# Optimization experiments

Measured on AMD Instinct MI355X. Metric: run time of the kernel, lower is better.

## Reference

```python
import jax, jax.numpy as jnp
import numpy as np

B, S, D, H = 2, 2048, 2048, 16
DH = D // H  # 128
EPS = 1e-6


def _rms_norm(x, w):
    # RMSNorm over last dim with learnable scale
    var = jnp.mean(jnp.square(x), axis=-1, keepdims=True)
    return x * jax.lax.rsqrt(var + EPS) * w


def _apply_rope(x, angles):
    # x: [B, S, H, DH]; angles: [S, DH//2]; interleaved pair rotation
    xs = x.reshape(*x.shape[:-1], DH // 2, 2)
    x0, x1 = xs[..., 0], xs[..., 1]
    cos = jnp.cos(angles)[None, :, None, :]  # [1,S,1,DH/2]
    sin = jnp.sin(angles)[None, :, None, :]
    r0 = x0 * cos - x1 * sin
    r1 = x0 * sin + x1 * cos
    return jnp.stack([r0, r1], axis=-1).reshape(x.shape)


def setup_inputs() -> dict:
    key = jax.random.key(0)
    ks = jax.random.split(key, 4)
    x = jax.random.normal(ks[0], (B, S, D), dtype=jnp.float32)
    # standard RoPE angle table: pos * inv_freq
    inv_freq = 1.0 / (10000.0 ** (jnp.arange(0, DH, 2, dtype=jnp.float32) / DH))
    pos = jnp.arange(S, dtype=jnp.float32)
    rp_freqs = pos[:, None] * inv_freq[None, :]  # [S, DH/2]
    Win = jax.random.normal(ks[1], (3 * D, D), dtype=jnp.float32) * (D ** -0.5)
    b_in = jnp.zeros((3 * D,), dtype=jnp.float32)
    Wout = jax.random.normal(ks[2], (D, D), dtype=jnp.float32) * (D ** -0.5)
    b_out = jnp.zeros((D,), dtype=jnp.float32)
    qk_w = jnp.ones((DH,), dtype=jnp.float32)
    out_w = jnp.ones((D,), dtype=jnp.float32)
    return {"x": x, "rp_freqs": rp_freqs, "Win": Win, "b_in": b_in,
            "Wout": Wout, "b_out": b_out, "qk_w": qk_w, "out_w": out_w}


def reference(x, rp_freqs, Win, b_in, Wout, b_out, qk_w, out_w):
    b, s, d = x.shape
    qkv = jnp.einsum('bsd,ed->bse', x, Win) + b_in  # [B,S,3D]
    qkv = qkv.reshape(b, s, 3, H, DH)
    q, k, v = qkv[:, :, 0], qkv[:, :, 1], qkv[:, :, 2]  # each [B,S,H,DH]
    q = _apply_rope(q, rp_freqs)
    k = _apply_rope(k, rp_freqs)
    q = _rms_norm(q, qk_w)
    k = _rms_norm(k, qk_w)
    # causal SDPA, scale = 1/sqrt(DH) (default)
    a = jax.nn.dot_product_attention(q, k, v, is_causal=True)  # [B,S,H,DH]
    a = a.reshape(b, s, d)
    a = _rms_norm(a, out_w)
    return jnp.einsum('bsd,ed->bse', a, Wout) + b_out
```

## Files before the change

### kernel.cpp

```cpp
#include <hip/hip_runtime.h>
#include <cstdint>
#include <cstddef>

#define Bq  2
#define Sq  2048
#define Dq  2048
#define Hq  16
#define DHq 128
#define E3q 6144

typedef __attribute__((ext_vector_type(8))) short s16x8;
typedef __attribute__((ext_vector_type(4))) float f32x4;

__device__ __forceinline__ unsigned short f2bf(float f){
  union { float f; unsigned u; } v; v.f = f;
  unsigned r = v.u + 0x7FFFu + ((v.u >> 16) & 1u);
  return (unsigned short)(r >> 16);
}
__device__ __forceinline__ float bf2f(unsigned short b){
  union { unsigned u; float f; } v; v.u = ((unsigned)b) << 16;
  return v.f;
}
__device__ __forceinline__ unsigned cvtpk_bf16(float lo, float hi){
  unsigned r;
  asm("v_cvt_pk_bf16_f32 %0, %1, %2" : "=v"(r) : "v"(lo), "v"(hi));
  return r;
}

__device__ __forceinline__ void gload_lds16(const void* g, void* l){
  __builtin_amdgcn_global_load_lds(
      (const __attribute__((address_space(1))) void*)g,
      (__attribute__((address_space(3))) void*)l, 16, 0, 0);
}

__global__ __launch_bounds__(256) void k_convert(const float* __restrict__ in,
                                                 unsigned short* __restrict__ out, int n4){
  int stride = gridDim.x * blockDim.x;
  for (int i = blockIdx.x*blockDim.x + threadIdx.x; i < n4; i += stride){
    float4 v = reinterpret_cast<const float4*>(in)[i];
    ushort4 o;
    o.x = f2bf(v.x); o.y = f2bf(v.y); o.z = f2bf(v.z); o.w = f2bf(v.w);
    reinterpret_cast<ushort4*>(out)[i] = o;
  }
}

template<int F32OUT>
__global__ __launch_bounds__(512, 1) void k_gemm_bt(const unsigned short* __restrict__ A,
                                                    const unsigned short* __restrict__ Bt,
                                                    const float* __restrict__ bias,
                                                    void* __restrict__ C,
                                                    int M, int N, int K){
  const int bid = blockIdx.x;
  const int xcd = bid & 7, u = bid >> 3;
  const int by = xcd*4 + (u & 3);
  const int bx = u >> 2;
  const int m0 = by * 128, n0 = bx * 256;

  const int tid = threadIdx.x;
  const int w = tid >> 6, lane = tid & 63, g = lane >> 4, c = lane & 15;
  const int wm = w >> 2, wn = w & 3;

  __shared__ __align__(16) unsigned short L[6 * 12288];

  const int NT = K >> 5;

  const int arow = tid >> 2, apc = tid & 3;
  const int brow0 = tid >> 2, bpc0 = tid & 3;
  const int brow1 = (tid + 512) >> 2, bpc1 = tid & 3;
  const unsigned short* Abase  = &A [(size_t)(m0 + arow )*K + (size_t)((apc ^ ((arow >>1)&3))*8)];
  const unsigned short* Bbase0 = &Bt[(size_t)(n0 + brow0)*K + (size_t)((bpc0 ^ ((brow0>>1)&3))*8)];
  const unsigned short* Bbase1 = &Bt[(size_t)(n0 + brow1)*K + (size_t)((bpc1 ^ ((brow1>>1)&3))*8)];

  auto stage = [&](int tile, int slot){
    const int kt = tile << 5;
    unsigned short* Ls = &L[slot * 12288];
    gload_lds16(Abase  + kt, &Ls[tid*8]);
    gload_lds16(Bbase0 + kt, &Ls[4096 + tid*8]);
    gload_lds16(Bbase1 + kt, &Ls[4096 + (tid+512)*8]);
  };

  f32x4 acc[4][4];
#pragma unroll
  for (int i=0;i<4;i++)
#pragma unroll
    for (int j=0;j<4;j++)
#pragma unroll
      for (int r=0;r<4;r++) acc[i][j][r] = 0.f;

  int aoff[4], boff[4];
#pragma unroll
  for (int mi=0;mi<4;mi++){
    int row = wm*64 + mi*16 + c;
    aoff[mi] = row*32 + ((g ^ ((row>>1)&3)) << 3);
  }
#pragma unroll
  for (int ni=0;ni<4;ni++){
    int row = wn*64 + ni*16 + c;
    boff[ni] = 4096 + row*32 + ((g ^ ((row>>1)&3)) << 3);
  }

  stage(0,0); stage(1,1); stage(2,2); stage(3,3); stage(4,4);

  int slot = 0;
  for (int t = 0; t < NT; ++t){
    const int rem = NT-1-t;
    if (rem >= 4)      asm volatile("s_waitcnt vmcnt(12)" ::: "memory");
    else if (rem == 3) asm volatile("s_waitcnt vmcnt(9)"  ::: "memory");
    else if (rem == 2) asm volatile("s_waitcnt vmcnt(6)"  ::: "memory");
    else if (rem == 1) asm volatile("s_waitcnt vmcnt(3)"  ::: "memory");
    else               asm volatile("s_waitcnt vmcnt(0)"  ::: "memory");
    __builtin_amdgcn_s_barrier();
    __builtin_amdgcn_sched_barrier(0);
    if (t+5 < NT) stage(t+5, slot == 0 ? 5 : slot-1);

    const unsigned short* Ls = &L[slot * 12288];
    s16x8 bfr[4];
#pragma unroll
    for (int ni=0;ni<4;ni++) bfr[ni] = *(const s16x8*)&Ls[boff[ni]];
    __builtin_amdgcn_s_setprio(1);
#pragma unroll
    for (int mi=0;mi<4;mi++){
      s16x8 af = *(const s16x8*)&Ls[aoff[mi]];
#pragma unroll
      for (int ni=0;ni<4;ni++)
        acc[mi][ni] = __builtin_amdgcn_mfma_f32_16x16x32_bf16(af, bfr[ni], acc[mi][ni], 0,0,0);
    }
    __builtin_amdgcn_s_setprio(0);
    slot = (slot == 5) ? 0 : slot+1;
  }

#pragma unroll
  for (int ni=0;ni<4;ni++){
    const int col = n0 + wn*64 + ni*16 + c;
    const float bv = bias[col];
#pragma unroll
    for (int mi=0;mi<4;mi++){
      const int row = m0 + wm*64 + mi*16 + g*4;
#pragma unroll
      for (int r=0;r<4;r++){
        float v = acc[mi][ni][r] + bv;
        if (F32OUT) ((float*)C)[(size_t)(row+r)*N + col] = v;
        else ((unsigned short*)C)[(size_t)(row+r)*N + col] = f2bf(v);
      }
    }
  }
}

__global__ __launch_bounds__(256) void k_rope_qk(const unsigned short* __restrict__ QKV,
                                                 const float* __restrict__ rp,
                                                 const float* __restrict__ qk_w,
                                                 unsigned short* __restrict__ Qp,
                                                 unsigned short* __restrict__ Kp){
  const int p = threadIdx.x;
  const int s = blockIdx.x*4 + threadIdx.y;
  const int h = blockIdx.y;
  const int b = blockIdx.z;
  const size_t n = (size_t)b*Sq + s;
  const int bh = b*Hq + h;

  float ang = rp[s*64 + p];
  float sn, cs; sincosf(ang, &sn, &cs);
  float w0 = qk_w[2*p], w1 = qk_w[2*p+1];
  const float QSCALE = 0.08838834764831845f * 1.4426950408889634f;

  {
    unsigned q01 = *(const unsigned*)&QKV[n*E3q + h*DHq + 2*p];
    float x0 = bf2f((unsigned short)(q01 & 0xFFFFu));
    float x1 = bf2f((unsigned short)(q01 >> 16));
    float r0 = x0*cs - x1*sn, r1 = x0*sn + x1*cs;
    float ss = r0*r0 + r1*r1;
#pragma unroll
    for (int m=1;m<64;m<<=1) ss += __shfl_xor(ss, m);
    float sc = rsqrtf(ss/128.f + 1e-6f) * QSCALE;
    unsigned short o0 = f2bf(r0*sc*w0), o1 = f2bf(r1*sc*w1);
    *(unsigned*)&Qp[((size_t)bh*Sq + s)*DHq + 2*p] = (unsigned)o0 | ((unsigned)o1<<16);
  }
  {
    unsigned k01 = *(const unsigned*)&QKV[n*E3q + Dq + h*DHq + 2*p];
    float x0 = bf2f((unsigned short)(k01 & 0xFFFFu));
    float x1 = bf2f((unsigned short)(k01 >> 16));
    float r0 = x0*cs - x1*sn, r1 = x0*sn + x1*cs;
    float ss = r0*r0 + r1*r1;
#pragma unroll
    for (int m=1;m<64;m<<=1) ss += __shfl_xor(ss, m);
    float sc = rsqrtf(ss/128.f + 1e-6f);
    unsigned short o0 = f2bf(r0*sc*w0), o1 = f2bf(r1*sc*w1);
    *(unsigned*)&Kp[((size_t)bh*Sq + s)*DHq + 2*p] = (unsigned)o0 | ((unsigned)o1<<16);
  }
}

__global__ __launch_bounds__(256) void k_transpose_v(const unsigned short* __restrict__ QKV,
                                                     unsigned short* __restrict__ Vt){
  const int sblk = blockIdx.x;
  const int bh = blockIdx.y;
  const int b = bh >> 4, h = bh & 15;
  const int tid = threadIdx.x;
  __shared__ unsigned short T[128][136];

  const size_t base = ((size_t)(b*Sq) + sblk*128) * E3q + 2*(size_t)Dq + h*DHq;
#pragma unroll
  for (int i=0;i<8;i++){
    int pk = tid + i*256;
    int row = pk >> 4, cc = (pk & 15) * 8;
    s16x8 v = *(const s16x8*)&QKV[base + (size_t)row*E3q + cc];
    *(s16x8*)&T[row][cc] = v;
  }
  __syncthreads();
  const int dh = tid >> 1, sh = (tid & 1) * 64;
  unsigned short buf[64];
#pragma unroll
  for (int s=0;s<64;s++) buf[s] = T[sh + s][dh];
  size_t obase = ((size_t)bh*DHq + dh)*Sq + sblk*128 + sh;
#pragma unroll
  for (int i=0;i<8;i++)
    *(s16x8*)&Vt[obase + i*8] = *(const s16x8*)&buf[i*8];
}

__global__ __launch_bounds__(256, 2) void k_attn(const unsigned short* __restrict__ Qp,
                                                 const unsigned short* __restrict__ Kp,
                                                 const unsigned short* __restrict__ Vt,
                                                 unsigned short* __restrict__ Ar){
  const int L = blockIdx.x;
  int bh, qtile;
  if (L < 256){ bh = L >> 3; qtile = 8 + (L & 7); }
  else { int Ml = L - 256; bh = Ml >> 3; qtile = 7 - (Ml & 7); }
  const int b = bh >> 4, h = bh & 15;
  const int tid = threadIdx.x;
  const int w = tid >> 6, lane = tid & 63, g = lane >> 4, c = lane & 15;
  const int r0w = qtile*128 + w*32;

  const unsigned short* Qh = Qp + (size_t)bh * Sq * DHq;
  const unsigned short* Kh = Kp + (size_t)bh * Sq * DHq;
  const unsigned short* Vh = Vt + (size_t)bh * DHq * Sq;

  __shared__ __align__(16) unsigned short Ks[2][64*128];
  __shared__ __align__(16) unsigned short Vs[2][128*64];
  __shared__ __align__(16) unsigned short Pl[4][32*64];
  unsigned short* Pw = &Pl[w][0];

  s16x8 qf[2][4];
#pragma unroll
  for (int mi=0;mi<2;mi++)
#pragma unroll
    for (int kc=0;kc<4;kc++)
      qf[mi][kc] = *(const s16x8*)&Qh[(size_t)(r0w + mi*16 + c)*DHq + kc*32 + g*8];

  f32x4 acc[2][8];
#pragma unroll
  for (int mi=0;mi<2;mi++)
#pragma unroll
    for (int dt=0;dt<8;dt++)
#pragma unroll
      for (int r=0;r<4;r++) acc[mi][dt][r] = 0.f;
  float m_r[2] = { -INFINITY, -INFINITY };
  float l_p[2] = { 0.f, 0.f };

  const int nsteps = 2*qtile + 2;

  auto stage = [&](int j0s, int bufi){
#pragma unroll
    for (int i=0;i<4;i++){
      int pk = tid + i*256;
      int row = pk>>4, pc = pk&15;
      gload_lds16(&Kh[(size_t)(j0s+row)*DHq + ((pc^(row&7))<<3)], &Ks[bufi][pk*8]);
    }
#pragma unroll
    for (int i=0;i<4;i++){
      int pk = tid + i*256;
      int row = pk>>3, pc = pk&7;
      gload_lds16(&Vh[(size_t)row*Sq + j0s + ((pc^(row&7))<<3)], &Vs[bufi][pk*8]);
    }
  };

  stage(0, 0);
  __syncthreads();

  for (int t=0; t<nsteps; ++t){
    const int j0 = t*64;
    if (t+1 < nsteps) stage((t+1)*64, (t+1)&1);

    if (j0 <= r0w + 31){
      const unsigned short* Kc = &Ks[t&1][0];
      const unsigned short* Vc = &Vs[t&1][0];

      f32x4 sv[2][4];
#pragma unroll
      for (int mi=0;mi<2;mi++)
#pragma unroll
        for (int js=0;js<4;js++)
#pragma unroll
          for (int r=0;r<4;r++) sv[mi][js][r] = 0.f;

      __builtin_amdgcn_s_setprio(1);
#pragma unroll
      for (int js=0;js<4;js++){
        s16x8 kf[4];
#pragma unroll
        for (int kc=0;kc<4;kc++)
          kf[kc] = *(const s16x8*)&Kc[(js*16 + c)*128 + (((kc*4+g)^(c&7))<<3)];
#pragma unroll
        for (int mi=0;mi<2;mi++)
#pragma unroll
          for (int kc=0;kc<4;kc++)
            sv[mi][js] = __builtin_amdgcn_mfma_f32_16x16x32_bf16(kf[kc], qf[mi][kc], sv[mi][js], 0,0,0);
      }
      __builtin_amdgcn_s_setprio(0);

      if (j0 + 63 > r0w){
#pragma unroll
        for (int mi=0;mi<2;mi++){
          const int q = r0w + mi*16 + c;
#pragma unroll
          for (int js=0;js<4;js++)
#pragma unroll
            for (int r=0;r<4;r++)
              if (j0 + js*16 + g*4 + r > q) sv[mi][js][r] = -INFINITY;
        }
      }

      float pmx[2];
#pragma unroll
      for (int mi=0;mi<2;mi++){
        float mx = fmaxf(fmaxf(sv[mi][0][0],sv[mi][0][1]), fmaxf(sv[mi][0][2],sv[mi][0][3]));
#pragma unroll
        for (int js=1;js<4;js++){
          float a = fmaxf(fmaxf(sv[mi][js][0],sv[mi][js][1]), fmaxf(sv[mi][js][2],sv[mi][js][3]));
          mx = fmaxf(mx, a);
        }
        mx = fmaxf(mx, __shfl_xor(mx, 16));
        mx = fmaxf(mx, __shfl_xor(mx, 32));
        pmx[mi] = mx;
      }
      int need = (pmx[0] > m_r[0] + 8.f) | (pmx[1] > m_r[1] + 8.f);
      if (__any(need)){
#pragma unroll
        for (int mi=0;mi<2;mi++){
          float mnew = fmaxf(m_r[mi], pmx[mi]);
          float corr = exp2f(m_r[mi] - mnew);
          l_p[mi] *= corr;
          m_r[mi] = mnew;
#pragma unroll
          for (int dt=0;dt<8;dt++)
#pragma unroll
            for (int r=0;r<4;r++) acc[mi][dt][r] *= corr;
        }
      }
#pragma unroll
      for (int mi=0;mi<2;mi++){
        const float mm = m_r[mi];
        const int rowoff = (mi*16 + c)*64;
#pragma unroll
        for (int js=0;js<4;js++){
          float e0 = exp2f(sv[mi][js][0] - mm);
          float e1 = exp2f(sv[mi][js][1] - mm);
          float e2 = exp2f(sv[mi][js][2] - mm);
          float e3 = exp2f(sv[mi][js][3] - mm);
          l_p[mi] += (e0+e1)+(e2+e3);
          uint2 pk2;
          pk2.x = cvtpk_bf16(e0, e1);
          pk2.y = cvtpk_bf16(e2, e3);
          const int kc8 = js*2 + (g>>1);
          *(uint2*)&Pw[rowoff + ((kc8 ^ (c&7))<<3) + (g&1)*4] = pk2;
        }
      }

      s16x8 pfr[2][2];
#pragma unroll
      for (int mi=0;mi<2;mi++)
#pragma unroll
        for (int kc=0;kc<2;kc++)
          pfr[mi][kc] = *(const s16x8*)&Pw[(mi*16 + c)*64 + (((kc*4+g)^(c&7))<<3)];
      __builtin_amdgcn_s_setprio(1);
#pragma unroll
      for (int dt=0; dt<8; dt++){
#pragma unroll
        for (int kc=0;kc<2;kc++){
          s16x8 vfr = *(const s16x8*)&Vc[(dt*16 + c)*64 + (((kc*4+g)^(c&7))<<3)];
#pragma unroll
          for (int mi=0;mi<2;mi++)
            acc[mi][dt] = __builtin_amdgcn_mfma_f32_16x16x32_bf16(vfr, pfr[mi][kc], acc[mi][dt], 0,0,0);
        }
      }
      __builtin_amdgcn_s_setprio(0);
    }
    __syncthreads();
  }

#pragma unroll
  for (int mi=0;mi<2;mi++){
    float l = l_p[mi];
    l += __shfl_xor(l, 16);
    l += __shfl_xor(l, 32);
    const float inv = 1.f / l;
    const int row = r0w + mi*16 + c;
    unsigned short* dst = &Ar[((size_t)(b*Sq + row))*Dq + h*DHq];
#pragma unroll
    for (int dt=0; dt<8; dt++){
      uint2 o2;
      o2.x = cvtpk_bf16(acc[mi][dt][0]*inv, acc[mi][dt][1]*inv);
      o2.y = cvtpk_bf16(acc[mi][dt][2]*inv, acc[mi][dt][3]*inv);
      *(uint2*)&dst[dt*16 + g*4] = o2;
    }
  }
}

__global__ __launch_bounds__(256) void k_rmsnorm(unsigned short* __restrict__ A,
                                                 const float* __restrict__ w){
  const int row = blockIdx.x;
  const int tid = threadIdx.x;
  s16x8 v = *(const s16x8*)&A[(size_t)row*Dq + tid*8];
  float f[8]; float ss = 0.f;
#pragma unroll
  for (int i=0;i<8;i++){ f[i] = bf2f((unsigned short)v[i]); ss += f[i]*f[i]; }
#pragma unroll
  for (int m=1;m<64;m<<=1) ss += __shfl_xor(ss, m);
  __shared__ float red[4];
  if ((tid&63)==0) red[tid>>6] = ss;
  __syncthreads();
  ss = red[0]+red[1]+red[2]+red[3];
  float sc = rsqrtf(ss/2048.f + 1e-6f);
  unsigned short o[8];
#pragma unroll
  for (int i=0;i<8;i++) o[i] = f2bf(f[i]*sc*w[tid*8+i]);
  *(s16x8*)&A[(size_t)row*Dq + tid*8] = *(const s16x8*)o;
}

extern "C" void kernel_launch(void* const* d_in, const int* in_sizes, int n_in,
                              void* d_out, int out_size, void* d_ws, size_t ws_size,
                              hipStream_t stream){
  const float* x     = (const float*)d_in[0];
  const float* rp    = (const float*)d_in[1];
  const float* Win   = (const float*)d_in[2];
  const float* b_in  = (const float*)d_in[3];
  const float* Wout  = (const float*)d_in[4];
  const float* b_out = (const float*)d_in[5];
  const float* qk_w  = (const float*)d_in[6];
  const float* out_w = (const float*)d_in[7];
  float* outp = (float*)d_out;

  if (ws_size < (160ull<<20)) return;

  char* ws = (char*)d_ws;
  unsigned short* Xb    = (unsigned short*)(ws);
  unsigned short* Wb    = (unsigned short*)(ws + (16ull<<20));
  unsigned short* Woutb = (unsigned short*)(ws + (40ull<<20));
  unsigned short* QKVb  = (unsigned short*)(ws + (48ull<<20));
  unsigned short* Qp    = (unsigned short*)(ws + (96ull<<20));
  unsigned short* Kp    = (unsigned short*)(ws + (112ull<<20));
  unsigned short* Vt    = (unsigned short*)(ws + (128ull<<20));
  unsigned short* Ar    = (unsigned short*)(ws + (144ull<<20));

  k_convert<<<2048, 256, 0, stream>>>(x,    Xb,    (Bq*Sq*Dq)/4);
  k_convert<<<2048, 256, 0, stream>>>(Win,  Wb,    (E3q*Dq)/4);
  k_convert<<<1024, 256, 0, stream>>>(Wout, Woutb, (Dq*Dq)/4);
  k_gemm_bt<0><<<768, 512, 0, stream>>>(Xb, Wb, b_in, QKVb, Bq*Sq, E3q, Dq);
  k_rope_qk<<<dim3(Sq/4, Hq, Bq), dim3(64,4), 0, stream>>>(QKVb, rp, qk_w, Qp, Kp);
  k_transpose_v<<<dim3(Sq/128, Bq*Hq), 256, 0, stream>>>(QKVb, Vt);
  k_attn<<<512, 256, 0, stream>>>(Qp, Kp, Vt, Ar);
  k_rmsnorm<<<Bq*Sq, 256, 0, stream>>>(Ar, out_w);
  k_gemm_bt<1><<<256, 512, 0, stream>>>(Ar, Woutb, b_out, outp, Bq*Sq, Dq, Dq);
}
```

Measured before the change: 300.1 us.

## Restructure GEMM to 4 waves with 8x4 MFMA tiles and triple-buffered LDS

The GEMM block shrinks from 512 to 256 threads. Each wave now computes a 128x64 tile (8x4 MFMA accumulators), so A fragments are reused across more MFMAs. The LDS pipeline drops from 6 stages to 3, and launch bounds allow 2 blocks per CU so two workgroups can overlap each other's latency. The trade-off is a shallower prefetch depth and higher register pressure from 128 accumulator floats per lane.

```diff
diff --git a/kernel.cpp b/kernel.cpp
--- a/kernel.cpp
+++ b/kernel.cpp
@@ -45,7 +45,7 @@
 }
 
 template<int F32OUT>
-__global__ __launch_bounds__(512, 1) void k_gemm_bt(const unsigned short* __restrict__ A,
+__global__ __launch_bounds__(256, 2) void k_gemm_bt(const unsigned short* __restrict__ A,
                                                     const unsigned short* __restrict__ Bt,
                                                     const float* __restrict__ bias,
                                                     void* __restrict__ C,
@@ -58,60 +58,59 @@
 
   const int tid = threadIdx.x;
   const int w = tid >> 6, lane = tid & 63, g = lane >> 4, c = lane & 15;
-  const int wm = w >> 2, wn = w & 3;
-
-  __shared__ __align__(16) unsigned short L[6 * 12288];
+
+  __shared__ __align__(16) unsigned short L[3 * 12288];
 
   const int NT = K >> 5;
 
-  const int arow = tid >> 2, apc = tid & 3;
-  const int brow0 = tid >> 2, bpc0 = tid & 3;
-  const int brow1 = (tid + 512) >> 2, bpc1 = tid & 3;
-  const unsigned short* Abase  = &A [(size_t)(m0 + arow )*K + (size_t)((apc ^ ((arow >>1)&3))*8)];
-  const unsigned short* Bbase0 = &Bt[(size_t)(n0 + brow0)*K + (size_t)((bpc0 ^ ((brow0>>1)&3))*8)];
-  const unsigned short* Bbase1 = &Bt[(size_t)(n0 + brow1)*K + (size_t)((bpc1 ^ ((brow1>>1)&3))*8)];
+  const int r0 = tid >> 2, pc = tid & 3;
+  const unsigned short* Ab0 = &A [(size_t)(m0 + r0      )*K + (size_t)((pc ^ (((r0      )>>1)&3))*8)];
+  const unsigned short* Ab1 = &A [(size_t)(m0 + r0 +  64)*K + (size_t)((pc ^ (((r0 + 64)>>1)&3))*8)];
+  const unsigned short* Bb0 = &Bt[(size_t)(n0 + r0      )*K + (size_t)((pc ^ (((r0      )>>1)&3))*8)];
+  const unsigned short* Bb1 = &Bt[(size_t)(n0 + r0 +  64)*K + (size_t)((pc ^ (((r0 + 64)>>1)&3))*8)];
+  const unsigned short* Bb2 = &Bt[(size_t)(n0 + r0 + 128)*K + (size_t)((pc ^ (((r0 +128)>>1)&3))*8)];
+  const unsigned short* Bb3 = &Bt[(size_t)(n0 + r0 + 192)*K + (size_t)((pc ^ (((r0 +192)>>1)&3))*8)];
 
   auto stage = [&](int tile, int slot){
     const int kt = tile << 5;
     unsigned short* Ls = &L[slot * 12288];
-    gload_lds16(Abase  + kt, &Ls[tid*8]);
-    gload_lds16(Bbase0 + kt, &Ls[4096 + tid*8]);
-    gload_lds16(Bbase1 + kt, &Ls[4096 + (tid+512)*8]);
+    gload_lds16(Ab0 + kt, &Ls[tid*8]);
+    gload_lds16(Ab1 + kt, &Ls[(tid+256)*8]);
+    gload_lds16(Bb0 + kt, &Ls[4096 + tid*8]);
+    gload_lds16(Bb1 + kt, &Ls[4096 + (tid+256)*8]);
+    gload_lds16(Bb2 + kt, &Ls[4096 + (tid+512)*8]);
+    gload_lds16(Bb3 + kt, &Ls[4096 + (tid+768)*8]);
   };
 
-  f32x4 acc[4][4];
-#pragma unroll
-  for (int i=0;i<4;i++)
+  f32x4 acc[8][4];
+#pragma unroll
+  for (int i=0;i<8;i++)
 #pragma unroll
     for (int j=0;j<4;j++)
 #pragma unroll
       for (int r=0;r<4;r++) acc[i][j][r] = 0.f;
 
-  int aoff[4], boff[4];
-#pragma unroll
-  for (int mi=0;mi<4;mi++){
-    int row = wm*64 + mi*16 + c;
+  int aoff[8], boff[4];
+#pragma unroll
+  for (int mi=0;mi<8;mi++){
+    int row = mi*16 + c;
     aoff[mi] = row*32 + ((g ^ ((row>>1)&3)) << 3);
   }
 #pragma unroll
   for (int ni=0;ni<4;ni++){
-    int row = wn*64 + ni*16 + c;
+    int row = w*64 + ni*16 + c;
     boff[ni] = 4096 + row*32 + ((g ^ ((row>>1)&3)) << 3);
   }
 
-  stage(0,0); stage(1,1); stage(2,2); stage(3,3); stage(4,4);
+  stage(0,0); stage(1,1);
 
   int slot = 0;
   for (int t = 0; t < NT; ++t){
-    const int rem = NT-1-t;
-    if (rem >= 4)      asm volatile("s_waitcnt vmcnt(12)" ::: "memory");
-    else if (rem == 3) asm volatile("s_waitcnt vmcnt(9)"  ::: "memory");
-    else if (rem == 2) asm volatile("s_waitcnt vmcnt(6)"  ::: "memory");
-    else if (rem == 1) asm volatile("s_waitcnt vmcnt(3)"  ::: "memory");
-    else               asm volatile("s_waitcnt vmcnt(0)"  ::: "memory");
+    if (t < NT-1) asm volatile("s_waitcnt vmcnt(6)" ::: "memory");
+    else          asm volatile("s_waitcnt vmcnt(0)" ::: "memory");
     __builtin_amdgcn_s_barrier();
     __builtin_amdgcn_sched_barrier(0);
-    if (t+5 < NT) stage(t+5, slot == 0 ? 5 : slot-1);
+    if (t+2 < NT) stage(t+2, slot == 0 ? 2 : slot-1);
 
     const unsigned short* Ls = &L[slot * 12288];
     s16x8 bfr[4];
@@ -119,23 +118,23 @@
     for (int ni=0;ni<4;ni++) bfr[ni] = *(const s16x8*)&Ls[boff[ni]];
     __builtin_amdgcn_s_setprio(1);
 #pragma unroll
-    for (int mi=0;mi<4;mi++){
+    for (int mi=0;mi<8;mi++){
       s16x8 af = *(const s16x8*)&Ls[aoff[mi]];
 #pragma unroll
       for (int ni=0;ni<4;ni++)
         acc[mi][ni] = __builtin_amdgcn_mfma_f32_16x16x32_bf16(af, bfr[ni], acc[mi][ni], 0,0,0);
     }
     __builtin_amdgcn_s_setprio(0);
-    slot = (slot == 5) ? 0 : slot+1;
+    slot = (slot == 2) ? 0 : slot+1;
   }
 
 #pragma unroll
   for (int ni=0;ni<4;ni++){
-    const int col = n0 + wn*64 + ni*16 + c;
+    const int col = n0 + w*64 + ni*16 + c;
     const float bv = bias[col];
 #pragma unroll
-    for (int mi=0;mi<4;mi++){
-      const int row = m0 + wm*64 + mi*16 + g*4;
+    for (int mi=0;mi<8;mi++){
+      const int row = m0 + mi*16 + g*4;
 #pragma unroll
       for (int r=0;r<4;r++){
         float v = acc[mi][ni][r] + bv;
@@ -261,14 +260,14 @@
 #pragma unroll
     for (int i=0;i<4;i++){
       int pk = tid + i*256;
-      int row = pk>>4, pc = pk&15;
-      gload_lds16(&Kh[(size_t)(j0s+row)*DHq + ((pc^(row&7))<<3)], &Ks[bufi][pk*8]);
+      int row = pk>>4, pcc = pk&15;
+      gload_lds16(&Kh[(size_t)(j0s+row)*DHq + ((pcc^(row&7))<<3)], &Ks[bufi][pk*8]);
     }
 #pragma unroll
     for (int i=0;i<4;i++){
       int pk = tid + i*256;
-      int row = pk>>3, pc = pk&7;
-      gload_lds16(&Vh[(size_t)row*Sq + j0s + ((pc^(row&7))<<3)], &Vs[bufi][pk*8]);
+      int row = pk>>3, pcc = pk&7;
+      gload_lds16(&Vh[(size_t)row*Sq + j0s + ((pcc^(row&7))<<3)], &Vs[bufi][pk*8]);
     }
   };
 
@@ -453,10 +452,10 @@
   k_convert<<<2048, 256, 0, stream>>>(x,    Xb,    (Bq*Sq*Dq)/4);
   k_convert<<<2048, 256, 0, stream>>>(Win,  Wb,    (E3q*Dq)/4);
   k_convert<<<1024, 256, 0, stream>>>(Wout, Woutb, (Dq*Dq)/4);
-  k_gemm_bt<0><<<768, 512, 0, stream>>>(Xb, Wb, b_in, QKVb, Bq*Sq, E3q, Dq);
+  k_gemm_bt<0><<<768, 256, 0, stream>>>(Xb, Wb, b_in, QKVb, Bq*Sq, E3q, Dq);
   k_rope_qk<<<dim3(Sq/4, Hq, Bq), dim3(64,4), 0, stream>>>(QKVb, rp, qk_w, Qp, Kp);
   k_transpose_v<<<dim3(Sq/128, Bq*Hq), 256, 0, stream>>>(QKVb, Vt);
   k_attn<<<512, 256, 0, stream>>>(Qp, Kp, Vt, Ar);
   k_rmsnorm<<<Bq*Sq, 256, 0, stream>>>(Ar, out_w);
-  k_gemm_bt<1><<<256, 512, 0, stream>>>(Ar, Woutb, b_out, outp, Bq*Sq, Dq, Dq);
-}
+  k_gemm_bt<1><<<256, 256, 0, stream>>>(Ar, Woutb, b_out, outp, Bq*Sq, Dq, Dq);
+}
```

Result: no change. 299.7 us (-0.1%).
